# Kernel optimization log

Hardware: AMD Instinct MI355X
Metric: run time of the kernel (lower is better)

The kernel has to match this reference:

```python
import jax, jax.numpy as jnp
import numpy as np

N_NODES = 100000


def setup_inputs() -> dict:
    key = jax.random.key(0)
    ks = jax.random.split(key, 6)
    d_in, d_hid, d_out = 128, 128, 128
    x = jax.random.normal(ks[0], (N_NODES, d_in), dtype=jnp.float32)
    # edge_index[0] = row (destination), edge_index[1] = col (source)
    edge_index = jax.random.randint(ks[1], (2, 1000000), 0, N_NODES, dtype=jnp.int64)
    W1 = jax.random.normal(ks[2], (2 * d_in, d_hid), dtype=jnp.float32) * (1.0 / np.sqrt(2 * d_in))
    b1 = jnp.zeros((d_hid,), dtype=jnp.float32)
    W2 = jax.random.normal(ks[3], (2 * d_hid, d_out), dtype=jnp.float32) * (1.0 / np.sqrt(2 * d_hid))
    b2 = jnp.zeros((d_out,), dtype=jnp.float32)
    return {"x": x, "edge_index": edge_index, "W1": W1, "b1": b1, "W2": W2, "b2": b2}


def _mean_aggregate(x, row, col, inv_deg):
    # out[i] = (1/deg(i)) * sum_{(i,j) in E} x[j]   (cogdl MeanAggregator: row_norm + spmm)
    agg = jax.ops.segment_sum(x[col], row, num_segments=x.shape[0])  # [N, d]
    return agg * inv_deg[:, None]


def _sage_layer(x, row, col, inv_deg, W, b):
    agg = _mean_aggregate(x, row, col, inv_deg)
    h = jnp.concatenate([x, agg], axis=-1)  # [N, 2d]
    return h @ W + b


def reference(x, edge_index, W1, b1, W2, b2):
    row, col = edge_index[0], edge_index[1]
    n = x.shape[0]
    deg = jax.ops.segment_sum(jnp.ones(row.shape, dtype=x.dtype), row, num_segments=n)
    inv_deg = jnp.where(deg > 0, 1.0 / jnp.maximum(deg, 1.0), 0.0).astype(x.dtype)
    h = jax.nn.relu(_sage_layer(x, row, col, inv_deg, W1, b1))
    # (dropout omitted: deterministic/eval reference)
    out = _sage_layer(h, row, col, inv_deg, W2, b2)
    return out
```

## Files before the change

kernel.cpp:

```cpp
#include <hip/hip_runtime.h>

#define D 128
#define MAXDEG 64
#define BIN_SHIFT 7
#define BINCAP 2048
#define EPB 8192

typedef short short8 __attribute__((ext_vector_type(8)));
typedef short short4v __attribute__((ext_vector_type(4)));
typedef float float4v __attribute__((ext_vector_type(4)));

__device__ __forceinline__ unsigned short f2bf(float f) {
    union { float f; unsigned u; } v; v.f = f;
    unsigned r = v.u + 0x7FFFu + ((v.u >> 16) & 1u);
    return (unsigned short)(r >> 16);
}
__device__ __forceinline__ float bflo(unsigned p) {
    union { unsigned u; float f; } v; v.u = p << 16; return v.f;
}
__device__ __forceinline__ float bfhi(unsigned p) {
    union { unsigned u; float f; } v; v.u = p & 0xFFFF0000u; return v.f;
}

__global__ __launch_bounds__(1024) void prep_kernel(const int* __restrict__ row,
                                                    const int* __restrict__ col,
                                                    int* __restrict__ bincnt,
                                                    long long* __restrict__ binbuf,
                                                    int nE, int nbins, int binGrid,
                                                    const float2* __restrict__ x,
                                                    unsigned* __restrict__ xb, int nPairs,
                                                    const float* __restrict__ W1,
                                                    const float* __restrict__ W2,
                                                    unsigned short* __restrict__ Wt1,
                                                    unsigned short* __restrict__ Wt2,
                                                    unsigned* __restrict__ hb, int n) {
    __shared__ int bcnt[1024];
    __shared__ int bbase[1024];
    const int t = threadIdx.x;

    if (blockIdx.x < (unsigned)binGrid) {
        const int e0 = blockIdx.x * EPB + t * 8;
        if (t < nbins) bcnt[t] = 0;
        __syncthreads();

        int rr[8], cc[8], bin[8], pos[8];
        if (e0 + 8 <= nE) {
            int4 r0 = *(const int4*)&row[e0];
            int4 r1 = *(const int4*)&row[e0 + 4];
            int4 c0 = *(const int4*)&col[e0];
            int4 c1 = *(const int4*)&col[e0 + 4];
            rr[0] = r0.x; rr[1] = r0.y; rr[2] = r0.z; rr[3] = r0.w;
            rr[4] = r1.x; rr[5] = r1.y; rr[6] = r1.z; rr[7] = r1.w;
            cc[0] = c0.x; cc[1] = c0.y; cc[2] = c0.z; cc[3] = c0.w;
            cc[4] = c1.x; cc[5] = c1.y; cc[6] = c1.z; cc[7] = c1.w;
            #pragma unroll
            for (int k = 0; k < 8; ++k) {
                bin[k] = rr[k] >> BIN_SHIFT;
                pos[k] = atomicAdd(&bcnt[bin[k]], 1);
            }
        } else {
            #pragma unroll
            for (int k = 0; k < 8; ++k) {
                int e = e0 + k;
                if (e < nE) {
                    rr[k] = row[e]; cc[k] = col[e];
                    bin[k] = rr[k] >> BIN_SHIFT;
                    pos[k] = atomicAdd(&bcnt[bin[k]], 1);
                } else { pos[k] = -1; bin[k] = 0; rr[k] = 0; cc[k] = 0; }
            }
        }
        __syncthreads();

        if (t < nbins) {
            int c = bcnt[t];
            bbase[t] = (c > 0) ? atomicAdd(&bincnt[t << 4], c) : 0;
        }
        __syncthreads();

        #pragma unroll
        for (int k = 0; k < 8; ++k) {
            if (pos[k] >= 0) {
                int slot = bbase[bin[k]] + pos[k];
                if (slot < BINCAP)
                    binbuf[(size_t)bin[k] * BINCAP + slot] =
                        ((long long)cc[k] << 32) | (unsigned)rr[k];
            }
        }
    } else if (blockIdx.x < (unsigned)(binGrid + 64)) {
        int id = (blockIdx.x - binGrid) * 1024 + t;
        int e = id & 32767;
        int c = e >> 8, k = e & 255;
        if (id < 32768) Wt1[c * 256 + k] = f2bf(W1[k * 128 + c]);
        else            Wt2[c * 256 + k] = f2bf(W2[k * 128 + c]);
    } else {
        int cb = blockIdx.x - binGrid - 64;
        if (cb == 0 && t < 64) {
            xb[((size_t)n << 6) + t] = 0;
            hb[((size_t)n << 6) + t] = 0;
        }
        int id = cb * 1024 + t;
        int stride = (gridDim.x - binGrid - 64) * 1024;
        for (int i = id; i < nPairs; i += stride) {
            float2 v = x[i];
            xb[i] = (unsigned)f2bf(v.x) | ((unsigned)f2bf(v.y) << 16);
        }
    }
}

__global__ __launch_bounds__(256) void ellbuild_kernel(const long long* __restrict__ binbuf,
                                                       const int* __restrict__ bincnt,
                                                       int* __restrict__ cnt,
                                                       int* __restrict__ bucket, int n) {
    __shared__ int lcnt[1 << BIN_SHIFT];
    const int b = blockIdx.x, t = threadIdx.x;
    const int base = b << BIN_SHIFT;
    if (t < (1 << BIN_SHIFT)) lcnt[t] = 0;
    __syncthreads();
    int m = bincnt[b << 4];
    if (m > BINCAP) m = BINCAP;
    const long long* buf = binbuf + (size_t)b * BINCAP;
    for (int j = t; j < m; j += 256) {
        long long pk = buf[j];
        int r = (int)pk;
        int c = (int)(pk >> 32);
        int pos = atomicAdd(&lcnt[r - base], 1);
        if (pos < MAXDEG) bucket[((size_t)r << 6) + pos] = c;
    }
    __syncthreads();
    if (t < (1 << BIN_SHIFT)) {
        int node = base + t;
        if (node < n) {
            int c0 = lcnt[t];
            cnt[node] = c0;
            int c = c0 > MAXDEG ? MAXDEG : c0;
            int cp = (c + 15) & ~15;
            for (int s = c; s < cp; ++s) bucket[((size_t)node << 6) + s] = n;
        }
    }
}

__device__ __forceinline__ void gather16(const unsigned* __restrict__ feat,
                                         const int* __restrict__ bk, int j, unsigned lane,
                                         float& x0, float& x1, float& x2, float& x3,
                                         float& y0, float& y1, float& y2, float& y3) {
    int4 c0 = *(const int4*)&bk[j];
    int4 c1 = *(const int4*)&bk[j + 4];
    int4 c2 = *(const int4*)&bk[j + 8];
    int4 c3 = *(const int4*)&bk[j + 12];
    unsigned v0  = feat[((unsigned)c0.x << 6) + lane];
    unsigned v1  = feat[((unsigned)c0.y << 6) + lane];
    unsigned v2  = feat[((unsigned)c0.z << 6) + lane];
    unsigned v3  = feat[((unsigned)c0.w << 6) + lane];
    unsigned v4  = feat[((unsigned)c1.x << 6) + lane];
    unsigned v5  = feat[((unsigned)c1.y << 6) + lane];
    unsigned v6  = feat[((unsigned)c1.z << 6) + lane];
    unsigned v7  = feat[((unsigned)c1.w << 6) + lane];
    unsigned v8  = feat[((unsigned)c2.x << 6) + lane];
    unsigned v9  = feat[((unsigned)c2.y << 6) + lane];
    unsigned v10 = feat[((unsigned)c2.z << 6) + lane];
    unsigned v11 = feat[((unsigned)c2.w << 6) + lane];
    unsigned v12 = feat[((unsigned)c3.x << 6) + lane];
    unsigned v13 = feat[((unsigned)c3.y << 6) + lane];
    unsigned v14 = feat[((unsigned)c3.z << 6) + lane];
    unsigned v15 = feat[((unsigned)c3.w << 6) + lane];
    x0 += bflo(v0);  y0 += bfhi(v0);
    x1 += bflo(v1);  y1 += bfhi(v1);
    x2 += bflo(v2);  y2 += bfhi(v2);
    x3 += bflo(v3);  y3 += bfhi(v3);
    x0 += bflo(v4);  y0 += bfhi(v4);
    x1 += bflo(v5);  y1 += bfhi(v5);
    x2 += bflo(v6);  y2 += bfhi(v6);
    x3 += bflo(v7);  y3 += bfhi(v7);
    x0 += bflo(v8);  y0 += bfhi(v8);
    x1 += bflo(v9);  y1 += bfhi(v9);
    x2 += bflo(v10); y2 += bfhi(v10);
    x3 += bflo(v11); y3 += bfhi(v11);
    x0 += bflo(v12); y0 += bfhi(v12);
    x1 += bflo(v13); y1 += bfhi(v13);
    x2 += bflo(v14); y2 += bfhi(v14);
    x3 += bflo(v15); y3 += bfhi(v15);
}

__global__ __launch_bounds__(256) void agg_bf16_kernel(const unsigned* __restrict__ feat,
                                                       const int* __restrict__ cnt,
                                                       const int* __restrict__ bucket,
                                                       unsigned* __restrict__ agg, int n) {
    long long tid = (long long)blockIdx.x * blockDim.x + threadIdx.x;
    int w = (int)(tid >> 6);
    int iA = w * 2, iB = w * 2 + 1;
    if (iA >= n) return;
    const unsigned lane = (unsigned)tid & 63u;

    int dtA = cnt[iA];
    int dA = dtA > MAXDEG ? MAXDEG : dtA;
    int dpA = (dA + 15) & ~15;
    int dtB = 0, dpB = 0;
    if (iB < n) {
        dtB = cnt[iB];
        int dB = dtB > MAXDEG ? MAXDEG : dtB;
        dpB = (dB + 15) & ~15;
    }
    const int* bkA = bucket + ((size_t)iA << 6);
    const int* bkB = bucket + ((size_t)iB << 6);

    float ax0=0,ax1=0,ax2=0,ax3=0, ay0=0,ay1=0,ay2=0,ay3=0;
    float bx0=0,bx1=0,bx2=0,bx3=0, by0=0,by1=0,by2=0,by3=0;
    int jm = dpA > dpB ? dpA : dpB;
    for (int j = 0; j < jm; j += 16) {
        if (j < dpA) gather16(feat, bkA, j, lane, ax0,ax1,ax2,ax3, ay0,ay1,ay2,ay3);
        if (j < dpB) gather16(feat, bkB, j, lane, bx0,bx1,bx2,bx3, by0,by1,by2,by3);
    }

    float invA = (dtA > 0) ? 1.0f / (float)dtA : 0.0f;
    float rxA = ((ax0 + ax1) + (ax2 + ax3)) * invA;
    float ryA = ((ay0 + ay1) + (ay2 + ay3)) * invA;
    agg[((size_t)iA << 6) + lane] = (unsigned)f2bf(rxA) | ((unsigned)f2bf(ryA) << 16);
    if (iB < n) {
        float invB = (dtB > 0) ? 1.0f / (float)dtB : 0.0f;
        float rxB = ((bx0 + bx1) + (bx2 + bx3)) * invB;
        float ryB = ((by0 + by1) + (by2 + by3)) * invB;
        agg[((size_t)iB << 6) + lane] = (unsigned)f2bf(rxB) | ((unsigned)f2bf(ryB) << 16);
    }
}

template <bool RELU, bool OUTF32>
__global__ __launch_bounds__(256) void sage_mfma(const unsigned short* __restrict__ selfb,
                                                 const unsigned short* __restrict__ aggb,
                                                 const unsigned short* __restrict__ Wtb,
                                                 const float* __restrict__ bias,
                                                 float* __restrict__ outf,
                                                 unsigned short* __restrict__ outb,
                                                 int n) {
    __shared__ short Alds[64 * 256];
    const int tid  = threadIdx.x;
    const int wave = tid >> 6;
    const int lane = tid & 63;
    const int r15  = lane & 15, g = lane >> 4;
    const int rowbase = blockIdx.x * 64;

    #pragma unroll
    for (int it = 0; it < 8; ++it) {
        int id  = it * 256 + tid;
        int row = id >> 5, cin = id & 31;
        int rowG = rowbase + row; if (rowG >= n) rowG = n - 1;
        const unsigned short* src = (cin < 16)
            ? selfb + (size_t)rowG * D + cin * 8
            : aggb  + (size_t)rowG * D + (cin - 16) * 8;
        int dchunk = cin ^ (row & 7);
        *(short8*)&Alds[row * 256 + dchunk * 8] = *(const short8*)src;
    }

    const int colbase = wave * 32;
    short8 bfr[2][8];
    #pragma unroll
    for (int cf = 0; cf < 2; ++cf) {
        const unsigned short* wp = Wtb + (size_t)(colbase + cf * 16 + r15) * 256;
        #pragma unroll
        for (int ks = 0; ks < 8; ++ks) {
            short4v lo = *(const short4v*)(wp + ks * 32 + 4 * g);
            short4v hi = *(const short4v*)(wp + ks * 32 + 16 + 4 * g);
            bfr[cf][ks] = __builtin_shufflevector(lo, hi, 0, 1, 2, 3, 4, 5, 6, 7);
        }
    }
    float bv0 = bias[colbase + r15];
    float bv1 = bias[colbase + 16 + r15];
    float4v acc[4][2];
    #pragma unroll
    for (int rf = 0; rf < 4; ++rf) {
        acc[rf][0] = (float4v){bv0, bv0, bv0, bv0};
        acc[rf][1] = (float4v){bv1, bv1, bv1, bv1};
    }

    __syncthreads();

    const int sw = (r15 & 7) << 4;
    #pragma unroll
    for (int ks = 0; ks < 8; ++ks) {
        #pragma unroll
        for (int rf = 0; rf < 4; ++rf) {
            const char* pr = (const char*)&Alds[(rf * 16 + r15) * 256];
            short4v lo = *(const short4v*)(pr + ((ks * 64 + 8 * g) ^ sw));
            short4v hi = *(const short4v*)(pr + ((ks * 64 + 8 * g + 32) ^ sw));
            short8 af = __builtin_shufflevector(lo, hi, 0, 1, 2, 3, 4, 5, 6, 7);
            acc[rf][0] = __builtin_amdgcn_mfma_f32_16x16x32_bf16(af, bfr[0][ks], acc[rf][0], 0, 0, 0);
            acc[rf][1] = __builtin_amdgcn_mfma_f32_16x16x32_bf16(af, bfr[1][ks], acc[rf][1], 0, 0, 0);
        }
    }

    if (OUTF32) {
        #pragma unroll
        for (int rf = 0; rf < 4; ++rf)
            #pragma unroll
            for (int cf = 0; cf < 2; ++cf)
                #pragma unroll
                for (int r = 0; r < 4; ++r) {
                    int row = rowbase + rf * 16 + g * 4 + r;
                    int col = colbase + cf * 16 + r15;
                    if (row < n) {
                        float v = acc[rf][cf][r];
                        if (RELU) v = (v > 0.0f) ? v : 0.0f;
                        outf[(size_t)row * D + col] = v;
                    }
                }
    } else {
        __syncthreads();
        unsigned short* ol = (unsigned short*)Alds;
        #pragma unroll
        for (int rf = 0; rf < 4; ++rf)
            #pragma unroll
            for (int cf = 0; cf < 2; ++cf)
                #pragma unroll
                for (int r = 0; r < 4; ++r) {
                    float v = acc[rf][cf][r];
                    if (RELU) v = (v > 0.0f) ? v : 0.0f;
                    ol[(rf * 16 + g * 4 + r) * 128 + colbase + cf * 16 + r15] = f2bf(v);
                }
        __syncthreads();
        #pragma unroll
        for (int it = 0; it < 4; ++it) {
            int id = it * 256 + tid;
            int r = id >> 4, ch = id & 15;
            int rowG = rowbase + r;
            if (rowG < n)
                *(short8*)&outb[(size_t)rowG * D + ch * 8] = *(const short8*)&ol[r * 128 + ch * 8];
        }
    }
}

extern "C" void kernel_launch(void* const* d_in, const int* in_sizes, int n_in,
                              void* d_out, int out_size, void* d_ws, size_t ws_size,
                              hipStream_t stream) {
    const float* x  = (const float*)d_in[0];
    const int*   ei = (const int*)d_in[1];
    const float* W1 = (const float*)d_in[2];
    const float* b1 = (const float*)d_in[3];
    const float* W2 = (const float*)d_in[4];
    const float* b2 = (const float*)d_in[5];
    float* out = (float*)d_out;

    const int n  = in_sizes[0] / D;
    const int nE = in_sizes[1] / 2;
    const int* row = ei;
    const int* col = ei + nE;
    const int nbins = (n + (1 << BIN_SHIFT) - 1) >> BIN_SHIFT;

    auto aup = [](size_t v) { return (v + 63) & ~(size_t)63; };
    int* wsI = (int*)d_ws;
    size_t o = 0;
    int* cnt    = wsI + o; o = aup(o + (size_t)n);
    int* bucket = wsI + o; o = aup(o + ((size_t)n << 6));
    unsigned* xb   = (unsigned*)(wsI + o); o = aup(o + (size_t)(n + 1) * 64);
    unsigned* hb   = (unsigned*)(wsI + o); o = aup(o + (size_t)(n + 1) * 64);
    unsigned* aggb = (unsigned*)(wsI + o); o = aup(o + (size_t)n * 64);
    unsigned short* Wt1 = (unsigned short*)(wsI + o); o = aup(o + 16384);
    unsigned short* Wt2 = (unsigned short*)(wsI + o); o = aup(o + 16384);
    int* bincnt = wsI + o; o = aup(o + (size_t)nbins * 16);
    long long* binbuf = (long long*)aggb;

    const int B = 256;
    const int binGrid = (nE + EPB - 1) / EPB;
    const int aggGrid = (int)((((long long)(n + 1) / 2) * 64 + B - 1) / B);
    const int mmGrid  = (n + 63) / 64;

    hipMemsetAsync(bincnt, 0, (size_t)nbins * 16 * sizeof(int), stream);
    prep_kernel<<<binGrid + 64 + 512, 1024, 0, stream>>>(
        row, col, bincnt, binbuf, nE, nbins, binGrid,
        (const float2*)x, xb, n * 64, W1, W2, Wt1, Wt2, hb, n);
    ellbuild_kernel<<<nbins, B, 0, stream>>>(binbuf, bincnt, cnt, bucket, n);

    agg_bf16_kernel<<<aggGrid, B, 0, stream>>>(xb, cnt, bucket, aggb, n);
    sage_mfma<true, false><<<mmGrid, B, 0, stream>>>(
        (const unsigned short*)xb, (const unsigned short*)aggb, Wt1, b1,
        nullptr, (unsigned short*)hb, n);

    agg_bf16_kernel<<<aggGrid, B, 0, stream>>>(hb, cnt, bucket, aggb, n);
    sage_mfma<false, true><<<mmGrid, B, 0, stream>>>(
        (const unsigned short*)hb, (const unsigned short*)aggb, Wt2, b2,
        out, nullptr, n);
}
```

Baseline: 194.2 us.

## Make MFMA SAGE GEMM persistent with register-prefetched next tile

The dense SAGE GEMM kernel becomes persistent: a grid of at most 768 blocks loops over 64-row tiles. Each block loads the weight fragments into registers once and reuses them across tiles. The next tile's A data is prefetched into registers while the current tile's MFMAs run. A separate LDS buffer is added for the bf16 output staging. This removes repeated weight loads and hides global load latency, at the cost of more registers and LDS, which may reduce occupancy.

```diff
diff --git a/kernel.cpp b/kernel.cpp
--- a/kernel.cpp
+++ b/kernel.cpp
@@ -230,25 +230,13 @@
                                                  const float* __restrict__ bias,
                                                  float* __restrict__ outf,
                                                  unsigned short* __restrict__ outb,
-                                                 int n) {
+                                                 int n, int ntiles) {
     __shared__ short Alds[64 * 256];
+    __shared__ unsigned short Olds[64 * 128];
     const int tid  = threadIdx.x;
     const int wave = tid >> 6;
     const int lane = tid & 63;
     const int r15  = lane & 15, g = lane >> 4;
-    const int rowbase = blockIdx.x * 64;
-
-    #pragma unroll
-    for (int it = 0; it < 8; ++it) {
-        int id  = it * 256 + tid;
-        int row = id >> 5, cin = id & 31;
-        int rowG = rowbase + row; if (rowG >= n) rowG = n - 1;
-        const unsigned short* src = (cin < 16)
-            ? selfb + (size_t)rowG * D + cin * 8
-            : aggb  + (size_t)rowG * D + (cin - 16) * 8;
-        int dchunk = cin ^ (row & 7);
-        *(short8*)&Alds[row * 256 + dchunk * 8] = *(const short8*)src;
-    }
 
     const int colbase = wave * 32;
     short8 bfr[2][8];
@@ -262,67 +250,98 @@
             bfr[cf][ks] = __builtin_shufflevector(lo, hi, 0, 1, 2, 3, 4, 5, 6, 7);
         }
     }
-    float bv0 = bias[colbase + r15];
-    float bv1 = bias[colbase + 16 + r15];
-    float4v acc[4][2];
-    #pragma unroll
-    for (int rf = 0; rf < 4; ++rf) {
-        acc[rf][0] = (float4v){bv0, bv0, bv0, bv0};
-        acc[rf][1] = (float4v){bv1, bv1, bv1, bv1};
-    }
-
-    __syncthreads();
-
+    const float bv0 = bias[colbase + r15];
+    const float bv1 = bias[colbase + 16 + r15];
+
+    short8 areg[8];
+    auto loadA = [&](int t) {
+        int rowbase = t * 64;
+        #pragma unroll
+        for (int it = 0; it < 8; ++it) {
+            int id  = it * 256 + tid;
+            int row = id >> 5, cin = id & 31;
+            int rowG = rowbase + row; if (rowG >= n) rowG = n - 1;
+            const unsigned short* src = (cin < 16)
+                ? selfb + (size_t)rowG * D + cin * 8
+                : aggb  + (size_t)rowG * D + (cin - 16) * 8;
+            areg[it] = *(const short8*)src;
+        }
+    };
+
+    int tile = blockIdx.x;
+    if (tile < ntiles) loadA(tile);
     const int sw = (r15 & 7) << 4;
-    #pragma unroll
-    for (int ks = 0; ks < 8; ++ks) {
+
+    for (; tile < ntiles; tile += gridDim.x) {
+        __syncthreads();
+        #pragma unroll
+        for (int it = 0; it < 8; ++it) {
+            int id  = it * 256 + tid;
+            int row = id >> 5, cin = id & 31;
+            int dch = cin ^ (row & 7);
+            *(short8*)&Alds[row * 256 + dch * 8] = areg[it];
+        }
+        __syncthreads();
+
+        int nt = tile + gridDim.x;
+        if (nt < ntiles) loadA(nt);
+
+        float4v acc[4][2];
         #pragma unroll
         for (int rf = 0; rf < 4; ++rf) {
-            const char* pr = (const char*)&Alds[(rf * 16 + r15) * 256];
-            short4v lo = *(const short4v*)(pr + ((ks * 64 + 8 * g) ^ sw));
-            short4v hi = *(const short4v*)(pr + ((ks * 64 + 8 * g + 32) ^ sw));
-            short8 af = __builtin_shufflevector(lo, hi, 0, 1, 2, 3, 4, 5, 6, 7);
-            acc[rf][0] = __builtin_amdgcn_mfma_f32_16x16x32_bf16(af, bfr[0][ks], acc[rf][0], 0, 0, 0);
-            acc[rf][1] = __builtin_amdgcn_mfma_f32_16x16x32_bf16(af, bfr[1][ks], acc[rf][1], 0, 0, 0);
-        }
-    }
-
-    if (OUTF32) {
-        #pragma unroll
-        for (int rf = 0; rf < 4; ++rf)
-            #pragma unroll
-            for (int cf = 0; cf < 2; ++cf)
+            acc[rf][0] = (float4v){bv0, bv0, bv0, bv0};
+            acc[rf][1] = (float4v){bv1, bv1, bv1, bv1};
+        }
+
+        #pragma unroll
+        for (int ks = 0; ks < 8; ++ks) {
+            #pragma unroll
+            for (int rf = 0; rf < 4; ++rf) {
+                const char* pr = (const char*)&Alds[(rf * 16 + r15) * 256];
+                short4v lo = *(const short4v*)(pr + ((ks * 64 + 8 * g) ^ sw));
+                short4v hi = *(const short4v*)(pr + ((ks * 64 + 8 * g + 32) ^ sw));
+                short8 af = __builtin_shufflevector(lo, hi, 0, 1, 2, 3, 4, 5, 6, 7);
+                acc[rf][0] = __builtin_amdgcn_mfma_f32_16x16x32_bf16(af, bfr[0][ks], acc[rf][0], 0, 0, 0);
+                acc[rf][1] = __builtin_amdgcn_mfma_f32_16x16x32_bf16(af, bfr[1][ks], acc[rf][1], 0, 0, 0);
+            }
+        }
+
+        int rowbase = tile * 64;
+        if (OUTF32) {
+            #pragma unroll
+            for (int rf = 0; rf < 4; ++rf)
                 #pragma unroll
-                for (int r = 0; r < 4; ++r) {
-                    int row = rowbase + rf * 16 + g * 4 + r;
-                    int col = colbase + cf * 16 + r15;
-                    if (row < n) {
+                for (int cf = 0; cf < 2; ++cf)
+                    #pragma unroll
+                    for (int r = 0; r < 4; ++r) {
+                        int row = rowbase + rf * 16 + g * 4 + r;
+                        int col = colbase + cf * 16 + r15;
+                        if (row < n) {
+                            float v = acc[rf][cf][r];
+                            if (RELU) v = (v > 0.0f) ? v : 0.0f;
+                            outf[(size_t)row * D + col] = v;
+                        }
+                    }
+        } else {
+            #pragma unroll
+            for (int rf = 0; rf < 4; ++rf)
+                #pragma unroll
+                for (int cf = 0; cf < 2; ++cf)
+                    #pragma unroll
+                    for (int r = 0; r < 4; ++r) {
                         float v = acc[rf][cf][r];
                         if (RELU) v = (v > 0.0f) ? v : 0.0f;
-                        outf[(size_t)row * D + col] = v;
+                        Olds[(rf * 16 + g * 4 + r) * 128 + colbase + cf * 16 + r15] = f2bf(v);
                     }
-                }
-    } else {
-        __syncthreads();
-        unsigned short* ol = (unsigned short*)Alds;
-        #pragma unroll
-        for (int rf = 0; rf < 4; ++rf)
-            #pragma unroll
-            for (int cf = 0; cf < 2; ++cf)
-                #pragma unroll
-                for (int r = 0; r < 4; ++r) {
-                    float v = acc[rf][cf][r];
-                    if (RELU) v = (v > 0.0f) ? v : 0.0f;
-                    ol[(rf * 16 + g * 4 + r) * 128 + colbase + cf * 16 + r15] = f2bf(v);
-                }
-        __syncthreads();
-        #pragma unroll
-        for (int it = 0; it < 4; ++it) {
-            int id = it * 256 + tid;
-            int r = id >> 4, ch = id & 15;
-            int rowG = rowbase + r;
-            if (rowG < n)
-                *(short8*)&outb[(size_t)rowG * D + ch * 8] = *(const short8*)&ol[r * 128 + ch * 8];
+            __syncthreads();
+            #pragma unroll
+            for (int it = 0; it < 4; ++it) {
+                int id = it * 256 + tid;
+                int r = id >> 4, ch = id & 15;
+                int rowG = rowbase + r;
+                if (rowG < n)
+                    *(short8*)&outb[(size_t)rowG * D + ch * 8] = *(const short8*)&Olds[r * 128 + ch * 8];
+            }
         }
     }
 }
@@ -360,7 +379,8 @@
     const int B = 256;
     const int binGrid = (nE + EPB - 1) / EPB;
     const int aggGrid = (int)((((long long)(n + 1) / 2) * 64 + B - 1) / B);
-    const int mmGrid  = (n + 63) / 64;
+    const int ntiles  = (n + 63) / 64;
+    const int mmGrid  = ntiles < 768 ? ntiles : 768;
 
     hipMemsetAsync(bincnt, 0, (size_t)nbins * 16 * sizeof(int), stream);
     prep_kernel<<<binGrid + 64 + 512, 1024, 0, stream>>>(
@@ -371,10 +391,10 @@
     agg_bf16_kernel<<<aggGrid, B, 0, stream>>>(xb, cnt, bucket, aggb, n);
     sage_mfma<true, false><<<mmGrid, B, 0, stream>>>(
         (const unsigned short*)xb, (const unsigned short*)aggb, Wt1, b1,
-        nullptr, (unsigned short*)hb, n);
+        nullptr, (unsigned short*)hb, n, ntiles);
 
     agg_bf16_kernel<<<aggGrid, B, 0, stream>>>(hb, cnt, bucket, aggb, n);
     sage_mfma<false, true><<<mmGrid, B, 0, stream>>>(
         (const unsigned short*)hb, (const unsigned short*)aggb, Wt2, b2,
-        out, nullptr, n);
-}
+        out, nullptr, n, ntiles);
+}
```

Result: faster. 169.3 us (-12.9%).
